# Kernel tuning notes

Hardware: AMD Instinct MI355X
Metric: run time of the kernel (lower is better)

## Reference

```python
import jax, jax.numpy as jnp
import numpy as np

B, T, D, U = 32, 512, 512, 512

def hard_sigmoid(x):
    return jnp.clip(0.2 * x + 0.5, 0.0, 1.0)

def gru_scan(x_seq, W, U_rec, b):
    """Classic GRU (reset_after=False) scanned over time.
    x_seq: [B,T,D]; W: [D,3U]; U_rec: [U,3U]; b: [3U].
    Returns (last_state [B,U], outputs [B,T,U] in scan order)."""
    u = U_rec.shape[0]
    Uzr = U_rec[:, :2 * u]   # recurrent weights for z, r gates
    Uh = U_rec[:, 2 * u:]    # recurrent weights for candidate
    x_gates = jnp.einsum('btd,dk->btk', x_seq, W) + b  # [B,T,3U] precomputed input proj

    def step(h, xg):
        xz, xr, xh = jnp.split(xg, 3, axis=-1)
        hz, hr = jnp.split(h @ Uzr, 2, axis=-1)
        z = hard_sigmoid(xz + hz)
        r = hard_sigmoid(xr + hr)
        cand = jnp.tanh(xh + (r * h) @ Uh)
        h_new = z * h + (1.0 - z) * cand
        return h_new, h_new

    h0 = jnp.zeros((x_seq.shape[0], u), dtype=x_seq.dtype)
    hT, outs = jax.lax.scan(step, h0, jnp.swapaxes(x_gates, 0, 1))
    return hT, jnp.swapaxes(outs, 0, 1)

def setup_inputs() -> dict:
    key = jax.random.key(0)
    ks = jax.random.split(key, 6)
    s_in = 1.0 / np.sqrt(D)
    s_rec = 1.0 / np.sqrt(U)
    return {
        'x':  jax.random.normal(ks[0], (B, T, D), dtype=jnp.float32),
        'Wf': jax.random.normal(ks[1], (D, 3 * U), dtype=jnp.float32) * s_in,
        'Uf': jax.random.normal(ks[2], (U, 3 * U), dtype=jnp.float32) * s_rec,
        'bf': jnp.zeros((3 * U,), dtype=jnp.float32),
        'Wb': jax.random.normal(ks[3], (D, 3 * U), dtype=jnp.float32) * s_in,
        'Ub': jax.random.normal(ks[4], (U, 3 * U), dtype=jnp.float32) * s_rec,
        'bb': jnp.zeros((3 * U,), dtype=jnp.float32),
    }

def reference(x, Wf, Uf, bf, Wb, Ub, bb):
    # forward direction
    _, outs_f = gru_scan(x, Wf, Uf, bf)
    # backward direction: K.rnn(go_backwards=True) processes reversed input and
    # AbstractBiRNN does NOT re-reverse outputs -> keep scan order.
    _, outs_b = gru_scan(x[:, ::-1, :], Wb, Ub, bb)
    # return_sequences=True -> concat per-timestep outputs along features
    return jnp.concatenate([outs_f, outs_b], axis=-1)  # [B,T,2U]
```

## Files before the change

kernel.cpp:

```cpp
#include <hip/hip_runtime.h>
#include <math.h>

#define BB 32
#define TT 512
#define DD 512
#define UU 512
#define G3 1536
#define CHUNK 64

__device__ __forceinline__ float hsig(float x) {
    return fminf(fmaxf(fmaf(0.2f, x, 0.5f), 0.0f), 1.0f);
}

__device__ __forceinline__ void llc_store_u64(unsigned long long* p,
                                              unsigned long long v) {
    __hip_atomic_store(p, v, __ATOMIC_RELAXED, __HIP_MEMORY_SCOPE_AGENT);
}
__device__ __forceinline__ unsigned long long pack_tv(unsigned tag, float v) {
    return ((unsigned long long)tag << 32) |
           (unsigned long long)__float_as_uint(v);
}

__global__ __launch_bounds__(256) void xg_gemm(
    const float* __restrict__ x,
    const float* __restrict__ Wf, const float* __restrict__ bf,
    const float* __restrict__ Wb, const float* __restrict__ bb,
    float* __restrict__ xgc, int t0)
{
    const int dir = blockIdx.z;
    const int n0  = blockIdx.x * 64;
    const int m0  = blockIdx.y * 128;
    const float* W    = dir ? Wb : Wf;
    const float* bias = dir ? bb : bf;

    __shared__ float As[16][132];
    __shared__ float Bs[16][64];

    const int tid = threadIdx.x;
    const int tx = tid & 15, ty = tid >> 4;

    float acc[8][4];
    #pragma unroll
    for (int i = 0; i < 8; ++i)
        #pragma unroll
        for (int q = 0; q < 4; ++q) acc[i][q] = 0.f;

    const int lmr = tid >> 2;
    const int ak4 = (tid & 3) * 4;
    const float* arow0;
    const float* arow1;
    {
        int m = m0 + lmr;
        int b = m & 31, i = m >> 5;
        int tp = dir ? (TT - 1 - t0 - i) : (t0 + i);
        arow0 = x + ((size_t)b * TT + tp) * DD;
        m = m0 + lmr + 64;
        b = m & 31; i = m >> 5;
        tp = dir ? (TT - 1 - t0 - i) : (t0 + i);
        arow1 = x + ((size_t)b * TT + tp) * DD;
    }
    const float* bsrc = W + (size_t)(tid >> 4) * G3 + n0 + (tid & 15) * 4;

    for (int k0 = 0; k0 < DD; k0 += 16) {
        float4 a0 = *(const float4*)(arow0 + k0 + ak4);
        float4 a1 = *(const float4*)(arow1 + k0 + ak4);
        float4 bv = *(const float4*)(bsrc + (size_t)k0 * G3);
        __syncthreads();
        As[ak4 + 0][lmr] = a0.x;  As[ak4 + 1][lmr] = a0.y;
        As[ak4 + 2][lmr] = a0.z;  As[ak4 + 3][lmr] = a0.w;
        As[ak4 + 0][lmr + 64] = a1.x;  As[ak4 + 1][lmr + 64] = a1.y;
        As[ak4 + 2][lmr + 64] = a1.z;  As[ak4 + 3][lmr + 64] = a1.w;
        *(float4*)&Bs[tid >> 4][(tid & 15) * 4] = bv;
        __syncthreads();
        #pragma unroll
        for (int kk = 0; kk < 16; ++kk) {
            float4 b4 = *(const float4*)&Bs[kk][tx * 4];
            #pragma unroll
            for (int i = 0; i < 8; ++i) {
                float a = As[kk][ty * 8 + i];
                acc[i][0] = fmaf(a, b4.x, acc[i][0]);
                acc[i][1] = fmaf(a, b4.y, acc[i][1]);
                acc[i][2] = fmaf(a, b4.z, acc[i][2]);
                acc[i][3] = fmaf(a, b4.w, acc[i][3]);
            }
        }
    }

    float4 bv = *(const float4*)(bias + n0 + tx * 4);
    #pragma unroll
    for (int i = 0; i < 8; ++i) {
        int m = m0 + ty * 8 + i;
        float4 o;
        o.x = acc[i][0] + bv.x;  o.y = acc[i][1] + bv.y;
        o.z = acc[i][2] + bv.z;  o.w = acc[i][3] + bv.w;
        *(float4*)(xgc + ((size_t)dir * (CHUNK * BB) + m) * G3 + n0 + tx * 4) = o;
    }
}

#define WSTRIDE 516
#define NWCOLS 48
#define P1S 264
#define P2S 132
#define LDS_FLOATS (NWCOLS * WSTRIDE + 8 * WSTRIDE + 9216 + 640)

__device__ __forceinline__ void stage_tagged(
    const unsigned long long* __restrict__ src,
    float* __restrict__ dst, int tid, unsigned exp)
{
    const unsigned long long* p0 = src + tid;
    const unsigned long long* p1 = src + tid + 512;
    const unsigned long long* p2 = src + tid + 1024;
    const unsigned long long* p3 = src + tid + 1536;
    const unsigned long long* p4 = src + tid + 2048;
    const unsigned long long* p5 = src + tid + 2560;
    const unsigned long long* p6 = src + tid + 3072;
    const unsigned long long* p7 = src + tid + 3584;
    unsigned long long d0, d1, d2, d3, d4, d5, d6, d7;
    for (int spin = 0;; ++spin) {
        asm volatile(
            "global_load_dwordx2 %0, %8, off sc0 sc1\n\t"
            "global_load_dwordx2 %1, %9, off sc0 sc1\n\t"
            "global_load_dwordx2 %2, %10, off sc0 sc1\n\t"
            "global_load_dwordx2 %3, %11, off sc0 sc1\n\t"
            "global_load_dwordx2 %4, %12, off sc0 sc1\n\t"
            "global_load_dwordx2 %5, %13, off sc0 sc1\n\t"
            "global_load_dwordx2 %6, %14, off sc0 sc1\n\t"
            "global_load_dwordx2 %7, %15, off sc0 sc1\n\t"
            "s_waitcnt vmcnt(0)"
            : "=&v"(d0), "=&v"(d1), "=&v"(d2), "=&v"(d3),
              "=&v"(d4), "=&v"(d5), "=&v"(d6), "=&v"(d7)
            : "v"(p0), "v"(p1), "v"(p2), "v"(p3),
              "v"(p4), "v"(p5), "v"(p6), "v"(p7)
            : "memory");
        unsigned bad = (((unsigned)(d0 >> 32)) ^ exp) |
                       (((unsigned)(d1 >> 32)) ^ exp) |
                       (((unsigned)(d2 >> 32)) ^ exp) |
                       (((unsigned)(d3 >> 32)) ^ exp) |
                       (((unsigned)(d4 >> 32)) ^ exp) |
                       (((unsigned)(d5 >> 32)) ^ exp) |
                       (((unsigned)(d6 >> 32)) ^ exp) |
                       (((unsigned)(d7 >> 32)) ^ exp);
        if (bad == 0u || spin > (1 << 18)) break;
        __builtin_amdgcn_s_sleep(1);
    }
    dst[tid]               = __uint_as_float((unsigned)d0);
    dst[WSTRIDE + tid]     = __uint_as_float((unsigned)d1);
    dst[2 * WSTRIDE + tid] = __uint_as_float((unsigned)d2);
    dst[3 * WSTRIDE + tid] = __uint_as_float((unsigned)d3);
    dst[4 * WSTRIDE + tid] = __uint_as_float((unsigned)d4);
    dst[5 * WSTRIDE + tid] = __uint_as_float((unsigned)d5);
    dst[6 * WSTRIDE + tid] = __uint_as_float((unsigned)d6);
    dst[7 * WSTRIDE + tid] = __uint_as_float((unsigned)d7);
}

__global__ __launch_bounds__(512, 1) void gru_chunk(
    const float* __restrict__ Uf, const float* __restrict__ Ub,
    const float* __restrict__ xgc,
    unsigned long long* __restrict__ hbuf,
    unsigned long long* __restrict__ rhbuf,
    float* __restrict__ out, int c)
{
    extern __shared__ float lds[];
    float* Wl   = lds;
    float* hp2  = lds;
    float* hp   = Wl + NWCOLS * WSTRIDE;
    float* part = hp + 8 * WSTRIDE;
    float* zloc = part + 9216;
    float* hloc = zloc + 128;
    float* xg_l = hloc + 128;

    const int tid = threadIdx.x;
    const int g   = blockIdx.x >> 5;
    const int w   = blockIdx.x & 31;
    const int dir = g >> 2;
    const int b0  = (g & 3) * 8;

    const float* U = dir ? Ub : Uf;
    const int j0 = w * 16;

    unsigned long long* hg_h[2];
    unsigned long long* hg_rh[2];
    hg_h[0]  = hbuf  + ((size_t)(0 * 2 + dir) * 32 + b0) * 512;
    hg_h[1]  = hbuf  + ((size_t)(1 * 2 + dir) * 32 + b0) * 512;
    hg_rh[0] = rhbuf + ((size_t)(0 * 2 + dir) * 32 + b0) * 512;
    hg_rh[1] = rhbuf + ((size_t)(1 * 2 + dir) * 32 + b0) * 512;

    for (int q = tid; q < 512 * 12; q += 512) {
        int k  = q & 511;
        int jj = q >> 9;
        int gate = jj >> 2;
        int off  = (jj & 3) * 4;
        int n  = gate * 512 + j0 + off;
        int cc = gate * 16 + off;
        float4 v = *(const float4*)(U + (size_t)k * G3 + n);
        float* wc = Wl + (size_t)cc * WSTRIDE + k;
        wc[0]           = v.x;
        wc[WSTRIDE]     = v.y;
        wc[2 * WSTRIDE] = v.z;
        wc[3 * WSTRIDE] = v.w;
    }
    __syncthreads();

    float4 w1[4][4];
    float4 w2[4][2];
    {
        const int cs1 = tid & 7, kb1 = (tid >> 4) * 16;
        #pragma unroll
        for (int ci = 0; ci < 4; ++ci)
            #pragma unroll
            for (int q = 0; q < 4; ++q)
                w1[ci][q] = *(const float4*)(Wl + (size_t)(cs1 + 8 * ci) * WSTRIDE
                                             + kb1 + 4 * q);
        const int cs2 = tid & 3, kb2 = (tid >> 3) * 8;
        #pragma unroll
        for (int ci = 0; ci < 4; ++ci)
            #pragma unroll
            for (int q = 0; q < 2; ++q)
                w2[ci][q] = *(const float4*)(Wl + (size_t)(32 + cs2 + 4 * ci) * WSTRIDE
                                             + kb2 + 4 * q);
    }
    __syncthreads();

    for (int i = 0; i < CHUNK; ++i) {
        const int t = c * CHUNK + i;
        const int par = t & 1;
        const unsigned tag_next = (unsigned)(t + 1);

        float xgv = 0.f;
        if (tid < 384) {
            size_t off;
            if (tid < 256) {
                off = (((size_t)dir * CHUNK + i) * BB + (b0 + (tid >> 5))) * G3
                    + (size_t)(((tid & 31) >> 4) * 512) + j0 + (tid & 15);
            } else {
                int o2 = tid - 256;
                off = (((size_t)dir * CHUNK + i) * BB + (b0 + (o2 >> 4))) * G3
                    + 1024 + j0 + (o2 & 15);
            }
            xgv = xgc[off];
        }

        stage_tagged(hg_h[par ^ 1], hp, tid, (unsigned)t);
        if (tid < 384) xg_l[tid] = xgv;
        __syncthreads();

        {
            const int cslot = tid & 7;
            const int bslot = (tid >> 3) & 1;
            const int ks    = tid >> 4;
            const int kb    = ks * 16;
            const float* hq = hp + (size_t)(bslot * 4) * WSTRIDE + kb;
            float acc[4][4];
            #pragma unroll
            for (int a = 0; a < 4; ++a)
                #pragma unroll
                for (int b = 0; b < 4; ++b) acc[a][b] = 0.f;
            #pragma unroll
            for (int q = 0; q < 4; ++q) {
                float4 hv[4];
                #pragma unroll
                for (int bi = 0; bi < 4; ++bi)
                    hv[bi] = *(const float4*)(hq + (size_t)bi * WSTRIDE + 4 * q);
                #pragma unroll
                for (int ci = 0; ci < 4; ++ci)
                    #pragma unroll
                    for (int bi = 0; bi < 4; ++bi) {
                        acc[ci][bi] = fmaf(w1[ci][q].x, hv[bi].x, acc[ci][bi]);
                        acc[ci][bi] = fmaf(w1[ci][q].y, hv[bi].y, acc[ci][bi]);
                        acc[ci][bi] = fmaf(w1[ci][q].z, hv[bi].z, acc[ci][bi]);
                        acc[ci][bi] = fmaf(w1[ci][q].w, hv[bi].w, acc[ci][bi]);
                    }
            }
            #pragma unroll
            for (int ci = 0; ci < 4; ++ci)
                #pragma unroll
                for (int bi = 0; bi < 4; ++bi) {
                    int o = (bslot * 4 + bi) * 32 + cslot + 8 * ci;
                    part[(size_t)ks * P1S + o] = acc[ci][bi];
                }
        }
        __syncthreads();

        if (tid < 256) {
            const int o = tid;
            float s0 = 0.f, s1 = 0.f, s2 = 0.f, s3 = 0.f;
            #pragma unroll
            for (int ks = 0; ks < 32; ks += 4) {
                s0 += part[(size_t)(ks + 0) * P1S + o];
                s1 += part[(size_t)(ks + 1) * P1S + o];
                s2 += part[(size_t)(ks + 2) * P1S + o];
                s3 += part[(size_t)(ks + 3) * P1S + o];
            }
            float s = ((s0 + s1) + (s2 + s3)) + xg_l[o];
            const int b_l = o >> 5, cc = o & 31;
            const int gate = cc >> 4;
            const int jl = cc & 15;
            const int j = j0 + jl;
            float gv = hsig(s);
            const float hval = hp[(size_t)b_l * WSTRIDE + j];
            if (gate == 0) {
                zloc[b_l * 16 + jl] = gv;
                hloc[b_l * 16 + jl] = hval;
            } else {
                llc_store_u64(hg_rh[par] + (size_t)b_l * 512 + j,
                              pack_tv(tag_next, gv * hval));
            }
        }

        stage_tagged(hg_rh[par], hp2, tid, tag_next);
        __syncthreads();

        {
            const int cslot = tid & 3;
            const int bslot = (tid >> 2) & 1;
            const int ks    = tid >> 3;
            const int kb    = ks * 8;
            const float* hq = hp2 + (size_t)(bslot * 4) * WSTRIDE + kb;
            float acc[4][4];
            #pragma unroll
            for (int a = 0; a < 4; ++a)
                #pragma unroll
                for (int b = 0; b < 4; ++b) acc[a][b] = 0.f;
            #pragma unroll
            for (int q = 0; q < 2; ++q) {
                float4 hv[4];
                #pragma unroll
                for (int bi = 0; bi < 4; ++bi)
                    hv[bi] = *(const float4*)(hq + (size_t)bi * WSTRIDE + 4 * q);
                #pragma unroll
                for (int ci = 0; ci < 4; ++ci)
                    #pragma unroll
                    for (int bi = 0; bi < 4; ++bi) {
                        acc[ci][bi] = fmaf(w2[ci][q].x, hv[bi].x, acc[ci][bi]);
                        acc[ci][bi] = fmaf(w2[ci][q].y, hv[bi].y, acc[ci][bi]);
                        acc[ci][bi] = fmaf(w2[ci][q].z, hv[bi].z, acc[ci][bi]);
                        acc[ci][bi] = fmaf(w2[ci][q].w, hv[bi].w, acc[ci][bi]);
                    }
            }
            #pragma unroll
            for (int ci = 0; ci < 4; ++ci)
                #pragma unroll
                for (int bi = 0; bi < 4; ++bi) {
                    int o = (bslot * 4 + bi) * 16 + cslot + 4 * ci;
                    part[(size_t)ks * P2S + o] = acc[ci][bi];
                }
        }
        __syncthreads();

        if (tid < 128) {
            const int o = tid;
            float s0 = 0.f, s1 = 0.f, s2 = 0.f, s3 = 0.f;
            #pragma unroll
            for (int ks = 0; ks < 64; ks += 4) {
                s0 += part[(size_t)(ks + 0) * P2S + o];
                s1 += part[(size_t)(ks + 1) * P2S + o];
                s2 += part[(size_t)(ks + 2) * P2S + o];
                s3 += part[(size_t)(ks + 3) * P2S + o];
            }
            float s = ((s0 + s1) + (s2 + s3)) + xg_l[256 + o];
            const int b_l = o >> 4, jl = o & 15;
            const int j = j0 + jl;
            float cand = tanhf(s);
            float z = zloc[b_l * 16 + jl];
            float h = hloc[b_l * 16 + jl];
            float hn = fmaf(z, h - cand, cand);
            llc_store_u64(hg_h[par] + (size_t)b_l * 512 + j,
                          pack_tv(tag_next, hn));
            out[((size_t)(b0 + b_l) * TT + t) * (2 * UU) + (size_t)dir * UU + j] = hn;
        }
        __syncthreads();
    }
}

extern "C" void kernel_launch(void* const* d_in, const int* in_sizes, int n_in,
                              void* d_out, int out_size, void* d_ws, size_t ws_size,
                              hipStream_t stream) {
    const float* x  = (const float*)d_in[0];
    const float* Wf = (const float*)d_in[1];
    const float* Uf = (const float*)d_in[2];
    const float* bf = (const float*)d_in[3];
    const float* Wb = (const float*)d_in[4];
    const float* Ub = (const float*)d_in[5];
    const float* bb = (const float*)d_in[6];
    float* out = (float*)d_out;

    unsigned long long* hbuf  = (unsigned long long*)d_ws;
    unsigned long long* rhbuf = hbuf + (size_t)4 * BB * UU;
    float* xgc = (float*)(rhbuf + (size_t)4 * BB * UU);

    hipMemsetAsync(d_ws, 0, (size_t)8 * 4 * BB * UU * 2, stream);

    static_assert(LDS_FLOATS * 4 <= 160 * 1024, "LDS overflow");
    hipFuncSetAttribute((const void*)gru_chunk,
                        hipFuncAttributeMaxDynamicSharedMemorySize,
                        LDS_FLOATS * 4);

    for (int c = 0; c < TT / CHUNK; ++c) {
        xg_gemm<<<dim3(24, 16, 2), 256, 0, stream>>>(
            x, Wf, bf, Wb, bb, xgc, c * CHUNK);
        gru_chunk<<<dim3(256), dim3(512), LDS_FLOATS * 4, stream>>>(
            Uf, Ub, xgc, hbuf, rhbuf, out, c);
    }
}
```

Measured before the change: 3.981 ms.

## Split each timestep into two 4-batch halves to overlap cross-block exchange

The 8-batch group handled by each block is split into two halves of 4 batches, and the recurrent step becomes four phases: z/r for half A, z/r for half B, candidate for half A, candidate for half B. Each phase stages only 4 rows of tagged global state. Work on one half can then proceed while the other half's exchanged values are still arriving, hiding part of the inter-block synchronization latency. The cost is twice as many block barriers and polling rounds per step, and thinner per-thread GEMV slices that need longer partial-sum reductions. LDS use also shrinks.

```diff
diff --git a/kernel.cpp b/kernel.cpp
--- a/kernel.cpp
+++ b/kernel.cpp
@@ -97,13 +97,12 @@
     }
 }
 
-#define WSTRIDE 516
-#define NWCOLS 48
-#define P1S 264
-#define P2S 132
-#define LDS_FLOATS (NWCOLS * WSTRIDE + 8 * WSTRIDE + 9216 + 640)
-
-__device__ __forceinline__ void stage_tagged(
+#define WST 516
+#define P1S2 136
+#define P2S2 68
+#define LDS_FLOATS (48 * WST + 640)
+
+__device__ __forceinline__ void stage_tagged4(
     const unsigned long long* __restrict__ src,
     float* __restrict__ dst, int tid, unsigned exp)
 {
@@ -111,46 +110,28 @@
     const unsigned long long* p1 = src + tid + 512;
     const unsigned long long* p2 = src + tid + 1024;
     const unsigned long long* p3 = src + tid + 1536;
-    const unsigned long long* p4 = src + tid + 2048;
-    const unsigned long long* p5 = src + tid + 2560;
-    const unsigned long long* p6 = src + tid + 3072;
-    const unsigned long long* p7 = src + tid + 3584;
-    unsigned long long d0, d1, d2, d3, d4, d5, d6, d7;
+    unsigned long long d0, d1, d2, d3;
     for (int spin = 0;; ++spin) {
         asm volatile(
-            "global_load_dwordx2 %0, %8, off sc0 sc1\n\t"
-            "global_load_dwordx2 %1, %9, off sc0 sc1\n\t"
-            "global_load_dwordx2 %2, %10, off sc0 sc1\n\t"
-            "global_load_dwordx2 %3, %11, off sc0 sc1\n\t"
-            "global_load_dwordx2 %4, %12, off sc0 sc1\n\t"
-            "global_load_dwordx2 %5, %13, off sc0 sc1\n\t"
-            "global_load_dwordx2 %6, %14, off sc0 sc1\n\t"
-            "global_load_dwordx2 %7, %15, off sc0 sc1\n\t"
+            "global_load_dwordx2 %0, %4, off sc0 sc1\n\t"
+            "global_load_dwordx2 %1, %5, off sc0 sc1\n\t"
+            "global_load_dwordx2 %2, %6, off sc0 sc1\n\t"
+            "global_load_dwordx2 %3, %7, off sc0 sc1\n\t"
             "s_waitcnt vmcnt(0)"
-            : "=&v"(d0), "=&v"(d1), "=&v"(d2), "=&v"(d3),
-              "=&v"(d4), "=&v"(d5), "=&v"(d6), "=&v"(d7)
-            : "v"(p0), "v"(p1), "v"(p2), "v"(p3),
-              "v"(p4), "v"(p5), "v"(p6), "v"(p7)
+            : "=&v"(d0), "=&v"(d1), "=&v"(d2), "=&v"(d3)
+            : "v"(p0), "v"(p1), "v"(p2), "v"(p3)
             : "memory");
         unsigned bad = (((unsigned)(d0 >> 32)) ^ exp) |
                        (((unsigned)(d1 >> 32)) ^ exp) |
                        (((unsigned)(d2 >> 32)) ^ exp) |
-                       (((unsigned)(d3 >> 32)) ^ exp) |
-                       (((unsigned)(d4 >> 32)) ^ exp) |
-                       (((unsigned)(d5 >> 32)) ^ exp) |
-                       (((unsigned)(d6 >> 32)) ^ exp) |
-                       (((unsigned)(d7 >> 32)) ^ exp);
+                       (((unsigned)(d3 >> 32)) ^ exp);
         if (bad == 0u || spin > (1 << 18)) break;
         __builtin_amdgcn_s_sleep(1);
     }
-    dst[tid]               = __uint_as_float((unsigned)d0);
-    dst[WSTRIDE + tid]     = __uint_as_float((unsigned)d1);
-    dst[2 * WSTRIDE + tid] = __uint_as_float((unsigned)d2);
-    dst[3 * WSTRIDE + tid] = __uint_as_float((unsigned)d3);
-    dst[4 * WSTRIDE + tid] = __uint_as_float((unsigned)d4);
-    dst[5 * WSTRIDE + tid] = __uint_as_float((unsigned)d5);
-    dst[6 * WSTRIDE + tid] = __uint_as_float((unsigned)d6);
-    dst[7 * WSTRIDE + tid] = __uint_as_float((unsigned)d7);
+    dst[tid]           = __uint_as_float((unsigned)d0);
+    dst[WST + tid]     = __uint_as_float((unsigned)d1);
+    dst[2 * WST + tid] = __uint_as_float((unsigned)d2);
+    dst[3 * WST + tid] = __uint_as_float((unsigned)d3);
 }
 
 __global__ __launch_bounds__(512, 1) void gru_chunk(
@@ -161,13 +142,16 @@
     float* __restrict__ out, int c)
 {
     extern __shared__ float lds[];
-    float* Wl   = lds;
-    float* hp2  = lds;
-    float* hp   = Wl + NWCOLS * WSTRIDE;
-    float* part = hp + 8 * WSTRIDE;
-    float* zloc = part + 9216;
-    float* hloc = zloc + 128;
-    float* xg_l = hloc + 128;
+    float* Wl    = lds;
+    float* hpA   = lds;
+    float* hpB   = lds + 4 * WST;
+    float* part  = lds + 8 * WST;
+    float* tail  = lds + 48 * WST;
+    float* zlocA = tail;
+    float* zlocB = tail + 64;
+    float* hlocA = tail + 128;
+    float* hlocB = tail + 192;
+    float* xg_l  = tail + 256;
 
     const int tid = threadIdx.x;
     const int g   = blockIdx.x >> 5;
@@ -193,33 +177,35 @@
         int n  = gate * 512 + j0 + off;
         int cc = gate * 16 + off;
         float4 v = *(const float4*)(U + (size_t)k * G3 + n);
-        float* wc = Wl + (size_t)cc * WSTRIDE + k;
-        wc[0]           = v.x;
-        wc[WSTRIDE]     = v.y;
-        wc[2 * WSTRIDE] = v.z;
-        wc[3 * WSTRIDE] = v.w;
+        float* wc = Wl + (size_t)cc * WST + k;
+        wc[0]       = v.x;
+        wc[WST]     = v.y;
+        wc[2 * WST] = v.z;
+        wc[3 * WST] = v.w;
     }
     __syncthreads();
 
-    float4 w1[4][4];
-    float4 w2[4][2];
+    float4 w1[4][2];
+    float4 w2[4];
     {
-        const int cs1 = tid & 7, kb1 = (tid >> 4) * 16;
+        const int cs1 = tid & 7, kb1 = (tid >> 3) * 8;
         #pragma unroll
         for (int ci = 0; ci < 4; ++ci)
             #pragma unroll
-            for (int q = 0; q < 4; ++q)
-                w1[ci][q] = *(const float4*)(Wl + (size_t)(cs1 + 8 * ci) * WSTRIDE
+            for (int q = 0; q < 2; ++q)
+                w1[ci][q] = *(const float4*)(Wl + (size_t)(cs1 + 8 * ci) * WST
                                              + kb1 + 4 * q);
-        const int cs2 = tid & 3, kb2 = (tid >> 3) * 8;
+        const int cs2 = tid & 3, kb2 = (tid >> 2) * 4;
         #pragma unroll
         for (int ci = 0; ci < 4; ++ci)
-            #pragma unroll
-            for (int q = 0; q < 2; ++q)
-                w2[ci][q] = *(const float4*)(Wl + (size_t)(32 + cs2 + 4 * ci) * WSTRIDE
-                                             + kb2 + 4 * q);
+            w2[ci] = *(const float4*)(Wl + (size_t)(32 + cs2 + 4 * ci) * WST + kb2);
     }
     __syncthreads();
+
+    const int cs1 = tid & 7;
+    const int ks1 = tid >> 3;
+    const int cs2 = tid & 3;
+    const int ks2 = tid >> 2;
 
     for (int i = 0; i < CHUNK; ++i) {
         const int t = c * CHUNK + i;
@@ -230,37 +216,36 @@
         if (tid < 384) {
             size_t off;
             if (tid < 256) {
-                off = (((size_t)dir * CHUNK + i) * BB + (b0 + (tid >> 5))) * G3
-                    + (size_t)(((tid & 31) >> 4) * 512) + j0 + (tid & 15);
+                int half = tid >> 7, o = tid & 127;
+                int b_l = o >> 5, cc = o & 31;
+                off = (((size_t)dir * CHUNK + i) * BB + (b0 + half * 4 + b_l)) * G3
+                    + (size_t)((cc >> 4) * 512) + j0 + (cc & 15);
             } else {
                 int o2 = tid - 256;
-                off = (((size_t)dir * CHUNK + i) * BB + (b0 + (o2 >> 4))) * G3
-                    + 1024 + j0 + (o2 & 15);
+                int half = o2 >> 6, o = o2 & 63;
+                off = (((size_t)dir * CHUNK + i) * BB + (b0 + half * 4 + (o >> 4))) * G3
+                    + 1024 + j0 + (o & 15);
             }
             xgv = xgc[off];
         }
 
-        stage_tagged(hg_h[par ^ 1], hp, tid, (unsigned)t);
+        stage_tagged4(hg_h[par ^ 1], hpA, tid, (unsigned)t);
         if (tid < 384) xg_l[tid] = xgv;
         __syncthreads();
 
         {
-            const int cslot = tid & 7;
-            const int bslot = (tid >> 3) & 1;
-            const int ks    = tid >> 4;
-            const int kb    = ks * 16;
-            const float* hq = hp + (size_t)(bslot * 4) * WSTRIDE + kb;
+            const float* hq = hpA + ks1 * 8;
             float acc[4][4];
             #pragma unroll
             for (int a = 0; a < 4; ++a)
                 #pragma unroll
                 for (int b = 0; b < 4; ++b) acc[a][b] = 0.f;
             #pragma unroll
-            for (int q = 0; q < 4; ++q) {
+            for (int q = 0; q < 2; ++q) {
                 float4 hv[4];
                 #pragma unroll
                 for (int bi = 0; bi < 4; ++bi)
-                    hv[bi] = *(const float4*)(hq + (size_t)bi * WSTRIDE + 4 * q);
+                    hv[bi] = *(const float4*)(hq + (size_t)bi * WST + 4 * q);
                 #pragma unroll
                 for (int ci = 0; ci < 4; ++ci)
                     #pragma unroll
@@ -274,48 +259,40 @@
             #pragma unroll
             for (int ci = 0; ci < 4; ++ci)
                 #pragma unroll
-                for (int bi = 0; bi < 4; ++bi) {
-                    int o = (bslot * 4 + bi) * 32 + cslot + 8 * ci;
-                    part[(size_t)ks * P1S + o] = acc[ci][bi];
-                }
-        }
-        __syncthreads();
-
-        if (tid < 256) {
+                for (int bi = 0; bi < 4; ++bi)
+                    part[(size_t)ks1 * P1S2 + bi * 32 + cs1 + 8 * ci] = acc[ci][bi];
+        }
+        __syncthreads();
+
+        if (tid < 128) {
             const int o = tid;
             float s0 = 0.f, s1 = 0.f, s2 = 0.f, s3 = 0.f;
             #pragma unroll
-            for (int ks = 0; ks < 32; ks += 4) {
-                s0 += part[(size_t)(ks + 0) * P1S + o];
-                s1 += part[(size_t)(ks + 1) * P1S + o];
-                s2 += part[(size_t)(ks + 2) * P1S + o];
-                s3 += part[(size_t)(ks + 3) * P1S + o];
+            for (int ks = 0; ks < 64; ks += 4) {
+                s0 += part[(size_t)(ks + 0) * P1S2 + o];
+                s1 += part[(size_t)(ks + 1) * P1S2 + o];
+                s2 += part[(size_t)(ks + 2) * P1S2 + o];
+                s3 += part[(size_t)(ks + 3) * P1S2 + o];
             }
             float s = ((s0 + s1) + (s2 + s3)) + xg_l[o];
             const int b_l = o >> 5, cc = o & 31;
-            const int gate = cc >> 4;
             const int jl = cc & 15;
             const int j = j0 + jl;
             float gv = hsig(s);
-            const float hval = hp[(size_t)b_l * WSTRIDE + j];
-            if (gate == 0) {
-                zloc[b_l * 16 + jl] = gv;
-                hloc[b_l * 16 + jl] = hval;
+            const float hval = hpA[(size_t)b_l * WST + j];
+            if (cc < 16) {
+                zlocA[b_l * 16 + jl] = gv;
+                hlocA[b_l * 16 + jl] = hval;
             } else {
                 llc_store_u64(hg_rh[par] + (size_t)b_l * 512 + j,
                               pack_tv(tag_next, gv * hval));
             }
         }
-
-        stage_tagged(hg_rh[par], hp2, tid, tag_next);
+        stage_tagged4(hg_h[par ^ 1] + 2048, hpB, tid, (unsigned)t);
         __syncthreads();
 
         {
-            const int cslot = tid & 3;
-            const int bslot = (tid >> 2) & 1;
-            const int ks    = tid >> 3;
-            const int kb    = ks * 8;
-            const float* hq = hp2 + (size_t)(bslot * 4) * WSTRIDE + kb;
+            const float* hq = hpB + ks1 * 8;
             float acc[4][4];
             #pragma unroll
             for (int a = 0; a < 4; ++a)
@@ -326,24 +303,22 @@
                 float4 hv[4];
                 #pragma unroll
                 for (int bi = 0; bi < 4; ++bi)
-                    hv[bi] = *(const float4*)(hq + (size_t)bi * WSTRIDE + 4 * q);
+                    hv[bi] = *(const float4*)(hq + (size_t)bi * WST + 4 * q);
                 #pragma unroll
                 for (int ci = 0; ci < 4; ++ci)
                     #pragma unroll
                     for (int bi = 0; bi < 4; ++bi) {
-                        acc[ci][bi] = fmaf(w2[ci][q].x, hv[bi].x, acc[ci][bi]);
-                        acc[ci][bi] = fmaf(w2[ci][q].y, hv[bi].y, acc[ci][bi]);
-                        acc[ci][bi] = fmaf(w2[ci][q].z, hv[bi].z, acc[ci][bi]);
-                        acc[ci][bi] = fmaf(w2[ci][q].w, hv[bi].w, acc[ci][bi]);
+                        acc[ci][bi] = fmaf(w1[ci][q].x, hv[bi].x, acc[ci][bi]);
+                        acc[ci][bi] = fmaf(w1[ci][q].y, hv[bi].y, acc[ci][bi]);
+                        acc[ci][bi] = fmaf(w1[ci][q].z, hv[bi].z, acc[ci][bi]);
+                        acc[ci][bi] = fmaf(w1[ci][q].w, hv[bi].w, acc[ci][bi]);
                     }
             }
             #pragma unroll
             for (int ci = 0; ci < 4; ++ci)
                 #pragma unroll
-                for (int bi = 0; bi < 4; ++bi) {
-                    int o = (bslot * 4 + bi) * 16 + cslot + 4 * ci;
-                    part[(size_t)ks * P2S + o] = acc[ci][bi];
-                }
+                for (int bi = 0; bi < 4; ++bi)
+                    part[(size_t)ks1 * P1S2 + bi * 32 + cs1 + 8 * ci] = acc[ci][bi];
         }
         __syncthreads();
 
@@ -352,21 +327,127 @@
             float s0 = 0.f, s1 = 0.f, s2 = 0.f, s3 = 0.f;
             #pragma unroll
             for (int ks = 0; ks < 64; ks += 4) {
-                s0 += part[(size_t)(ks + 0) * P2S + o];
-                s1 += part[(size_t)(ks + 1) * P2S + o];
-                s2 += part[(size_t)(ks + 2) * P2S + o];
-                s3 += part[(size_t)(ks + 3) * P2S + o];
+                s0 += part[(size_t)(ks + 0) * P1S2 + o];
+                s1 += part[(size_t)(ks + 1) * P1S2 + o];
+                s2 += part[(size_t)(ks + 2) * P1S2 + o];
+                s3 += part[(size_t)(ks + 3) * P1S2 + o];
+            }
+            float s = ((s0 + s1) + (s2 + s3)) + xg_l[128 + o];
+            const int b_l = o >> 5, cc = o & 31;
+            const int jl = cc & 15;
+            const int j = j0 + jl;
+            float gv = hsig(s);
+            const float hval = hpB[(size_t)b_l * WST + j];
+            if (cc < 16) {
+                zlocB[b_l * 16 + jl] = gv;
+                hlocB[b_l * 16 + jl] = hval;
+            } else {
+                llc_store_u64(hg_rh[par] + (size_t)(4 + b_l) * 512 + j,
+                              pack_tv(tag_next, gv * hval));
+            }
+        }
+        stage_tagged4(hg_rh[par], hpA, tid, tag_next);
+        __syncthreads();
+
+        {
+            const float* hq = hpA + ks2 * 4;
+            float acc[4][4];
+            #pragma unroll
+            for (int a = 0; a < 4; ++a)
+                #pragma unroll
+                for (int b = 0; b < 4; ++b) acc[a][b] = 0.f;
+            float4 hv[4];
+            #pragma unroll
+            for (int bi = 0; bi < 4; ++bi)
+                hv[bi] = *(const float4*)(hq + (size_t)bi * WST);
+            #pragma unroll
+            for (int ci = 0; ci < 4; ++ci)
+                #pragma unroll
+                for (int bi = 0; bi < 4; ++bi) {
+                    acc[ci][bi] = fmaf(w2[ci].x, hv[bi].x, acc[ci][bi]);
+                    acc[ci][bi] = fmaf(w2[ci].y, hv[bi].y, acc[ci][bi]);
+                    acc[ci][bi] = fmaf(w2[ci].z, hv[bi].z, acc[ci][bi]);
+                    acc[ci][bi] = fmaf(w2[ci].w, hv[bi].w, acc[ci][bi]);
+                }
+            #pragma unroll
+            for (int ci = 0; ci < 4; ++ci)
+                #pragma unroll
+                for (int bi = 0; bi < 4; ++bi)
+                    part[(size_t)ks2 * P2S2 + bi * 16 + cs2 + 4 * ci] = acc[ci][bi];
+        }
+        __syncthreads();
+
+        if (tid < 64) {
+            const int o = tid;
+            float s0 = 0.f, s1 = 0.f, s2 = 0.f, s3 = 0.f;
+            #pragma unroll
+            for (int ks = 0; ks < 128; ks += 4) {
+                s0 += part[(size_t)(ks + 0) * P2S2 + o];
+                s1 += part[(size_t)(ks + 1) * P2S2 + o];
+                s2 += part[(size_t)(ks + 2) * P2S2 + o];
+                s3 += part[(size_t)(ks + 3) * P2S2 + o];
             }
             float s = ((s0 + s1) + (s2 + s3)) + xg_l[256 + o];
             const int b_l = o >> 4, jl = o & 15;
             const int j = j0 + jl;
             float cand = tanhf(s);
-            float z = zloc[b_l * 16 + jl];
-            float h = hloc[b_l * 16 + jl];
+            float z = zlocA[o];
+            float h = hlocA[o];
             float hn = fmaf(z, h - cand, cand);
-            llc_store_u64(hg_h[par] + (size_t)b_l * 512 + j,
+            llc_store_u64(hg_h[par] + (size_t)b_l * 512 + j, pack_tv(tag_next, hn));
+            out[((size_t)(b0 + b_l) * TT + t) * (2 * UU) + (size_t)dir * UU + j] = hn;
+        }
+        stage_tagged4(hg_rh[par] + 2048, hpB, tid, tag_next);
+        __syncthreads();
+
+        {
+            const float* hq = hpB + ks2 * 4;
+            float acc[4][4];
+            #pragma unroll
+            for (int a = 0; a < 4; ++a)
+                #pragma unroll
+                for (int b = 0; b < 4; ++b) acc[a][b] = 0.f;
+            float4 hv[4];
+            #pragma unroll
+            for (int bi = 0; bi < 4; ++bi)
+                hv[bi] = *(const float4*)(hq + (size_t)bi * WST);
+            #pragma unroll
+            for (int ci = 0; ci < 4; ++ci)
+                #pragma unroll
+                for (int bi = 0; bi < 4; ++bi) {
+                    acc[ci][bi] = fmaf(w2[ci].x, hv[bi].x, acc[ci][bi]);
+                    acc[ci][bi] = fmaf(w2[ci].y, hv[bi].y, acc[ci][bi]);
+                    acc[ci][bi] = fmaf(w2[ci].z, hv[bi].z, acc[ci][bi]);
+                    acc[ci][bi] = fmaf(w2[ci].w, hv[bi].w, acc[ci][bi]);
+                }
+            #pragma unroll
+            for (int ci = 0; ci < 4; ++ci)
+                #pragma unroll
+                for (int bi = 0; bi < 4; ++bi)
+                    part[(size_t)ks2 * P2S2 + bi * 16 + cs2 + 4 * ci] = acc[ci][bi];
+        }
+        __syncthreads();
+
+        if (tid < 64) {
+            const int o = tid;
+            float s0 = 0.f, s1 = 0.f, s2 = 0.f, s3 = 0.f;
+            #pragma unroll
+            for (int ks = 0; ks < 128; ks += 4) {
+                s0 += part[(size_t)(ks + 0) * P2S2 + o];
+                s1 += part[(size_t)(ks + 1) * P2S2 + o];
+                s2 += part[(size_t)(ks + 2) * P2S2 + o];
+                s3 += part[(size_t)(ks + 3) * P2S2 + o];
+            }
+            float s = ((s0 + s1) + (s2 + s3)) + xg_l[320 + o];
+            const int b_l = o >> 4, jl = o & 15;
+            const int j = j0 + jl;
+            float cand = tanhf(s);
+            float z = zlocB[o];
+            float h = hlocB[o];
+            float hn = fmaf(z, h - cand, cand);
+            llc_store_u64(hg_h[par] + (size_t)(4 + b_l) * 512 + j,
                           pack_tv(tag_next, hn));
-            out[((size_t)(b0 + b_l) * TT + t) * (2 * UU) + (size_t)dir * UU + j] = hn;
+            out[((size_t)(b0 + 4 + b_l) * TT + t) * (2 * UU) + (size_t)dir * UU + j] = hn;
         }
         __syncthreads();
     }
```

Result: slower. 4.422 ms (+11.1%).
